# Performance work log

Hardware: AMD Instinct MI355X
Metric: run time of the kernel (lower is better)

## Reference

```python
import jax, jax.numpy as jnp
import numpy as np

N = 8192
SQUARE_SIZE = 10.0
NEIGHBOURHOOD = 1.0
THRESHOLD = 1.0
DECAY = 0.9


def setup_inputs() -> dict:
    key = jax.random.key(0)
    k1, k2, k3, k4 = jax.random.split(key, 4)
    # Random 2D topology on a square, as in SpikingLayer.__init__
    topo = jax.random.uniform(k1, (N, 2), dtype=jnp.float32) * SQUARE_SIZE
    # Pairwise squared distances without the [N,N,2] intermediate
    sq = jnp.sum(topo * topo, axis=1)  # [N]
    d2 = sq[:, None] + sq[None, :] - 2.0 * (topo @ topo.T)  # [N,N]
    mask = (d2 <= NEIGHBOURHOOD * NEIGHBOURHOOD).astype(jnp.float32)
    # Per-node weight rows, zeroed outside the neighbourhood radius
    W = jax.random.normal(k2, (N, N), dtype=jnp.float32) * mask
    # Random initial firing state (0/1) so dynamics are non-trivial
    f0 = (jax.random.uniform(k3, (N,)) > 0.5).astype(jnp.float32)
    v0 = jnp.zeros((N,), dtype=jnp.float32)
    x = jax.random.normal(k4, (N,), dtype=jnp.float32)  # unused, as in torch forward
    return {"W": W, "f0": f0, "v0": v0, "x": x, "num_steps": 64}


def reference(W, f0, v0, x, num_steps):
    # One scan step == one call to SpikingLayer.forward():
    #   node_x = W @ is_firing  (fused over all nodes)
    #   LIF update: v = decay*v + node_x; spike if v >= threshold; reset on spike
    def step(carry, _):
        v, f = carry
        u = W @ f                      # [N] weighted input from firing neighbours
        v = DECAY * v + u
        spike = v >= THRESHOLD         # bool [N]
        f_new = spike.astype(v.dtype)
        v = jnp.where(spike, 0.0, v)   # reset fired neurons
        return (v, f_new), f_new

    (_, _), firing_matrix = jax.lax.scan(step, (v0, f0), None, length=num_steps)
    return firing_matrix  # [num_steps, N], the accumulated firing_matrix
```

## Files before the change

kernel.cpp:

```cpp
#include <hip/hip_runtime.h>

#define NN 8192
#define STEPS 64
#define DECAYF 0.9f
#define THRESHF 1.0f
#define K_MAX 384
#define KITER2 (K_MAX / 32)

#define CBLOCKS 256
#define CTHREADS 1024
#define NWAVES 16
#define ROWS_PER_BLOCK 32

typedef unsigned long long u64;
typedef unsigned int u32;
typedef unsigned short u16;

__device__ __forceinline__ void pub_store(u64* p, u64 v) {
    __hip_atomic_store(p, v, __ATOMIC_RELAXED, __HIP_MEMORY_SCOPE_AGENT);
}
__device__ __forceinline__ u64 pub_load(const u64* p) {
    return __hip_atomic_load(p, __ATOMIC_RELAXED, __HIP_MEMORY_SCOPE_AGENT);
}

__global__ __launch_bounds__(CTHREADS) void spiking_all(
        const float* __restrict__ W,
        const float* __restrict__ f0,
        const float* __restrict__ v0,
        float* __restrict__ out,
        u64* __restrict__ fdata) {
    __shared__ u64 lds_pk[ROWS_PER_BLOCK * K_MAX];
    __shared__ u32 lds_fbits[2][CBLOCKS];
    __shared__ u32 lds_spike[NWAVES];
    __shared__ int lds_flag;
    __shared__ int lds_cnt[STEPS];

    const int tid  = threadIdx.x;
    const int wave = tid >> 6;
    const int lane = tid & 63;
    const int bid  = blockIdx.x;
    const u64 lmask = (1ull << lane) - 1ull;

    if (wave == 0) {
        float f = (lane < ROWS_PER_BLOCK) ? f0[bid * ROWS_PER_BLOCK + lane] : 0.0f;
        u64 m = __ballot(f != 0.0f);
        if (lane == 0)
            pub_store(&fdata[bid], (1ull << 32) | (u32)(m & 0xffffffffull));
    }

    for (int rr = 0; rr < 2; ++rr) {
        const int lr  = wave * 2 + rr;
        const int row = bid * ROWS_PER_BLOCK + lr;
        u64* pk = lds_pk + lr * K_MAX;
        for (int j = lane; j < K_MAX; j += 64) pk[j] = 0ull;
        const float4* wr4 = (const float4*)(W + (size_t)row * NN);
        int base = 0;
        for (int c4 = lane; c4 < NN / 4; c4 += 64) {
            float4 w = wr4[c4];
            const int col0 = c4 * 4;
            #pragma unroll
            for (int comp = 0; comp < 4; ++comp) {
                float val = (comp == 0) ? w.x : (comp == 1) ? w.y
                          : (comp == 2) ? w.z : w.w;
                u64 m = __ballot(val != 0.0f);
                if (val != 0.0f) {
                    int idx = base + __popcll(m & lmask);
                    if (idx < K_MAX)
                        pk[idx] = ((u64)(u32)(col0 + comp) << 32)
                                | (u64)__float_as_uint(val);
                }
                base += __popcll(m);
            }
        }
    }
    if (tid < STEPS) lds_cnt[tid] = 0;
    if (tid == 0) lds_flag = 0;

    const int lr   = wave * 2 + (lane >> 5);
    const int half = lane & 31;
    float vreg = v0[bid * ROWS_PER_BLOCK + lr];

    __syncthreads();

    for (int s = 0; s < STEPS; ++s) {
        if (wave == 0) {
            const u64* slot = fdata + (size_t)(s & 1) * CBLOCKS;
            const u32 want = (u32)(s + 1);
            u64 w0, w1, w2, w3;
            for (;;) {
                w0 = pub_load(&slot[lane]);
                w1 = pub_load(&slot[lane + 64]);
                w2 = pub_load(&slot[lane + 128]);
                w3 = pub_load(&slot[lane + 192]);
                int ok = ((u32)(w0 >> 32) == want) & ((u32)(w1 >> 32) == want)
                       & ((u32)(w2 >> 32) == want) & ((u32)(w3 >> 32) == want);
                if (__all(ok)) break;
            }
            u32* fb = lds_fbits[s & 1];
            fb[lane]       = (u32)w0;
            fb[lane + 64]  = (u32)w1;
            fb[lane + 128] = (u32)w2;
            fb[lane + 192] = (u32)w3;
            if (lane == 0)
                __hip_atomic_store(&lds_flag, s + 1, __ATOMIC_RELEASE,
                                   __HIP_MEMORY_SCOPE_WORKGROUP);
        } else {
            while (__hip_atomic_load(&lds_flag, __ATOMIC_ACQUIRE,
                                     __HIP_MEMORY_SCOPE_WORKGROUP) < s + 1)
                __builtin_amdgcn_s_sleep(1);
        }

        const u32* fb = lds_fbits[s & 1];
        const u64* pk = lds_pk + lr * K_MAX;

        double acc = 0.0;
        #pragma unroll
        for (int k = 0; k < KITER2; ++k) {
            const int j = half + (k << 5);
            u64 p   = pk[j];
            u32 c   = (u32)(p >> 32);
            float v = __uint_as_float((u32)p);
            u32 bit = (fb[c >> 5] >> (c & 31)) & 1u;
            acc += bit ? (double)v : 0.0;
        }
        #pragma unroll
        for (int m = 16; m >= 1; m >>= 1)
            acc += __shfl_xor(acc, m, 64);

        float u  = (float)acc;
        float vv = __fadd_rn(__fmul_rn(DECAYF, vreg), u);
        int fire = (vv >= THRESHF);
        vreg = fire ? 0.0f : vv;
        if (half == 0)
            out[(size_t)s * NN + bid * ROWS_PER_BLOCK + lr] = fire ? 1.0f : 0.0f;

        u64 bal = __ballot(fire);
        u32 bits2 = (u32)(bal & 1ull) | (u32)((bal >> 31) & 2ull);

        int old = -1;
        if (lane == 0) {
            __hip_atomic_store(&lds_spike[wave], bits2, __ATOMIC_RELAXED,
                               __HIP_MEMORY_SCOPE_WORKGROUP);
            old = __hip_atomic_fetch_add(&lds_cnt[s], 1, __ATOMIC_ACQ_REL,
                                         __HIP_MEMORY_SCOPE_WORKGROUP);
        }
        old = __shfl(old, 0, 64);
        if (old == NWAVES - 1) {
            u32 b = (lane < NWAVES) ? (lds_spike[lane] << (2 * lane)) : 0u;
            #pragma unroll
            for (int off = 8; off >= 1; off >>= 1)
                b |= __shfl_down(b, off, 64);
            if (lane == 0) {
                u64 word = ((u64)(u32)(s + 2) << 32) | b;
                pub_store(&fdata[(size_t)((s + 1) & 1) * CBLOCKS + bid], word);
            }
        }
    }
}

extern "C" void kernel_launch(void* const* d_in, const int* in_sizes, int n_in,
                              void* d_out, int out_size, void* d_ws, size_t ws_size,
                              hipStream_t stream) {
    const float* W  = (const float*)d_in[0];
    const float* f0 = (const float*)d_in[1];
    const float* v0 = (const float*)d_in[2];
    float* out = (float*)d_out;

    u64* fdata = (u64*)d_ws;

    spiking_all<<<dim3(CBLOCKS), dim3(CTHREADS), 0, stream>>>(W, f0, v0, out, fdata);
}
```

Before: 663.3 us.

## Split ELL extraction into separate kernel and hold sparse rows in registers

Moves the sparse-row extraction from the dense W matrix out of the persistent kernel into a separate kernel that is fully parallel over rows and writes a packed ELL array to the workspace. The persistent step kernel now uses 9 waves per block: one dedicated coordinator wave polls the global firing flags and publishes the block's spikes, and 8 compute waves each hold 4 rows' entries (24 per lane) in registers. This removes LDS staging of the packed entries and the per-step atomic counter election. The cost is an extra launch, a global round trip of the packed array, and a tighter coordinator-to-compute handshake through LDS.

```diff
diff --git a/kernel.cpp b/kernel.cpp
--- a/kernel.cpp
+++ b/kernel.cpp
@@ -5,16 +5,13 @@
 #define DECAYF 0.9f
 #define THRESHF 1.0f
 #define K_MAX 384
-#define KITER2 (K_MAX / 32)
+#define KITER 24
 
 #define CBLOCKS 256
-#define CTHREADS 1024
-#define NWAVES 16
-#define ROWS_PER_BLOCK 32
+#define STHREADS 576
 
 typedef unsigned long long u64;
 typedef unsigned int u32;
-typedef unsigned short u16;
 
 __device__ __forceinline__ void pub_store(u64* p, u64 v) {
     __hip_atomic_store(p, v, __ATOMIC_RELAXED, __HIP_MEMORY_SCOPE_AGENT);
@@ -23,67 +20,66 @@
     return __hip_atomic_load(p, __ATOMIC_RELAXED, __HIP_MEMORY_SCOPE_AGENT);
 }
 
-__global__ __launch_bounds__(CTHREADS) void spiking_all(
+__global__ __launch_bounds__(256) void extract_ell(
         const float* __restrict__ W,
+        u64* __restrict__ pk) {
+    const int wave = threadIdx.x >> 6;
+    const int lane = threadIdx.x & 63;
+    const int row  = blockIdx.x * 4 + wave;
+    const float4* wr4 = (const float4*)(W + (size_t)row * NN);
+    u64* pr = pk + (size_t)row * K_MAX;
+    const u64 lmask = (1ull << lane) - 1ull;
+
+    int base = 0;
+    for (int c4 = lane; c4 < NN / 4; c4 += 64) {
+        float4 w = wr4[c4];
+        const int col0 = c4 * 4;
+        #pragma unroll
+        for (int comp = 0; comp < 4; ++comp) {
+            float val = (comp == 0) ? w.x : (comp == 1) ? w.y
+                      : (comp == 2) ? w.z : w.w;
+            u64 m = __ballot(val != 0.0f);
+            if (val != 0.0f) {
+                int idx = base + __popcll(m & lmask);
+                if (idx < K_MAX)
+                    pr[idx] = ((u64)(u32)(col0 + comp) << 32)
+                            | (u64)__float_as_uint(val);
+            }
+            base += __popcll(m);
+        }
+    }
+    const int cap = (base < K_MAX) ? base : K_MAX;
+    for (int j = cap + lane; j < K_MAX; j += 64) pr[j] = 0ull;
+}
+
+__global__ __launch_bounds__(STHREADS) void spiking_steps(
+        const u64* __restrict__ pk,
         const float* __restrict__ f0,
         const float* __restrict__ v0,
         float* __restrict__ out,
         u64* __restrict__ fdata) {
-    __shared__ u64 lds_pk[ROWS_PER_BLOCK * K_MAX];
     __shared__ u32 lds_fbits[2][CBLOCKS];
-    __shared__ u32 lds_spike[NWAVES];
+    __shared__ u32 lds_spike[16];
     __shared__ int lds_flag;
-    __shared__ int lds_cnt[STEPS];
 
     const int tid  = threadIdx.x;
     const int wave = tid >> 6;
     const int lane = tid & 63;
     const int bid  = blockIdx.x;
-    const u64 lmask = (1ull << lane) - 1ull;
+
+    if (tid < 16) lds_spike[tid] = 0;
+    if (tid == 0) lds_flag = 0;
 
     if (wave == 0) {
-        float f = (lane < ROWS_PER_BLOCK) ? f0[bid * ROWS_PER_BLOCK + lane] : 0.0f;
+        float f = (lane < 32) ? f0[bid * 32 + lane] : 0.0f;
         u64 m = __ballot(f != 0.0f);
         if (lane == 0)
             pub_store(&fdata[bid], (1ull << 32) | (u32)(m & 0xffffffffull));
     }
-
-    for (int rr = 0; rr < 2; ++rr) {
-        const int lr  = wave * 2 + rr;
-        const int row = bid * ROWS_PER_BLOCK + lr;
-        u64* pk = lds_pk + lr * K_MAX;
-        for (int j = lane; j < K_MAX; j += 64) pk[j] = 0ull;
-        const float4* wr4 = (const float4*)(W + (size_t)row * NN);
-        int base = 0;
-        for (int c4 = lane; c4 < NN / 4; c4 += 64) {
-            float4 w = wr4[c4];
-            const int col0 = c4 * 4;
-            #pragma unroll
-            for (int comp = 0; comp < 4; ++comp) {
-                float val = (comp == 0) ? w.x : (comp == 1) ? w.y
-                          : (comp == 2) ? w.z : w.w;
-                u64 m = __ballot(val != 0.0f);
-                if (val != 0.0f) {
-                    int idx = base + __popcll(m & lmask);
-                    if (idx < K_MAX)
-                        pk[idx] = ((u64)(u32)(col0 + comp) << 32)
-                                | (u64)__float_as_uint(val);
-                }
-                base += __popcll(m);
-            }
-        }
-    }
-    if (tid < STEPS) lds_cnt[tid] = 0;
-    if (tid == 0) lds_flag = 0;
-
-    const int lr   = wave * 2 + (lane >> 5);
-    const int half = lane & 31;
-    float vreg = v0[bid * ROWS_PER_BLOCK + lr];
-
     __syncthreads();
 
-    for (int s = 0; s < STEPS; ++s) {
-        if (wave == 0) {
+    if (wave == 0) {
+        for (int s = 0; s < STEPS; ++s) {
             const u64* slot = fdata + (size_t)(s & 1) * CBLOCKS;
             const u32 want = (u32)(s + 1);
             u64 w0, w1, w2, w3;
@@ -104,55 +100,73 @@
             if (lane == 0)
                 __hip_atomic_store(&lds_flag, s + 1, __ATOMIC_RELEASE,
                                    __HIP_MEMORY_SCOPE_WORKGROUP);
-        } else {
+
+            u32 myw;
+            for (;;) {
+                myw = (lane < 8)
+                    ? __hip_atomic_load(&lds_spike[1 + lane], __ATOMIC_RELAXED,
+                                        __HIP_MEMORY_SCOPE_WORKGROUP)
+                    : (want << 8);
+                if (__all((myw >> 8) == want)) break;
+            }
+            u32 bits = (lane < 8) ? ((myw & 0xFu) << (lane * 4)) : 0u;
+            bits |= __shfl_xor(bits, 1, 64);
+            bits |= __shfl_xor(bits, 2, 64);
+            bits |= __shfl_xor(bits, 4, 64);
+            if (lane == 0)
+                pub_store(&fdata[(size_t)((s + 1) & 1) * CBLOCKS + bid],
+                          ((u64)(u32)(s + 2) << 32) | bits);
+        }
+    } else {
+        const int g    = wave - 1;
+        const int rloc = g * 4 + (lane >> 4);
+        const int row  = bid * 32 + rloc;
+        const int l16  = lane & 15;
+
+        u32 ecol[KITER]; float eval[KITER];
+        const u64* pr = pk + (size_t)row * K_MAX;
+        #pragma unroll
+        for (int k = 0; k < KITER; ++k) {
+            u64 p = pr[l16 + 16 * k];
+            ecol[k] = (u32)(p >> 32);
+            eval[k] = __uint_as_float((u32)p);
+        }
+        float vreg = v0[row];
+
+        for (int s = 0; s < STEPS; ++s) {
             while (__hip_atomic_load(&lds_flag, __ATOMIC_ACQUIRE,
                                      __HIP_MEMORY_SCOPE_WORKGROUP) < s + 1)
-                __builtin_amdgcn_s_sleep(1);
-        }
+                __builtin_amdgcn_s_sleep(2);
+            const u32* fb = lds_fbits[s & 1];
 
-        const u32* fb = lds_fbits[s & 1];
-        const u64* pk = lds_pk + lr * K_MAX;
+            double acc = 0.0;
+            #pragma unroll
+            for (int k = 0; k < KITER; ++k) {
+                u32 c = ecol[k];
+                u32 w = fb[c >> 5];
+                float sv = ((w >> (c & 31)) & 1u) ? eval[k] : 0.0f;
+                acc += (double)sv;
+            }
+            #pragma unroll
+            for (int m = 8; m >= 1; m >>= 1)
+                acc += __shfl_xor(acc, m, 64);
 
-        double acc = 0.0;
-        #pragma unroll
-        for (int k = 0; k < KITER2; ++k) {
-            const int j = half + (k << 5);
-            u64 p   = pk[j];
-            u32 c   = (u32)(p >> 32);
-            float v = __uint_as_float((u32)p);
-            u32 bit = (fb[c >> 5] >> (c & 31)) & 1u;
-            acc += bit ? (double)v : 0.0;
-        }
-        #pragma unroll
-        for (int m = 16; m >= 1; m >>= 1)
-            acc += __shfl_xor(acc, m, 64);
+            float u  = (float)acc;
+            float vv = __fadd_rn(__fmul_rn(DECAYF, vreg), u);
+            int fire = (vv >= THRESHF);
+            vreg = fire ? 0.0f : vv;
+            if (l16 == 0)
+                out[(size_t)s * NN + row] = fire ? 1.0f : 0.0f;
 
-        float u  = (float)acc;
-        float vv = __fadd_rn(__fmul_rn(DECAYF, vreg), u);
-        int fire = (vv >= THRESHF);
-        vreg = fire ? 0.0f : vv;
-        if (half == 0)
-            out[(size_t)s * NN + bid * ROWS_PER_BLOCK + lr] = fire ? 1.0f : 0.0f;
-
-        u64 bal = __ballot(fire);
-        u32 bits2 = (u32)(bal & 1ull) | (u32)((bal >> 31) & 2ull);
-
-        int old = -1;
-        if (lane == 0) {
-            __hip_atomic_store(&lds_spike[wave], bits2, __ATOMIC_RELAXED,
-                               __HIP_MEMORY_SCOPE_WORKGROUP);
-            old = __hip_atomic_fetch_add(&lds_cnt[s], 1, __ATOMIC_ACQ_REL,
-                                         __HIP_MEMORY_SCOPE_WORKGROUP);
-        }
-        old = __shfl(old, 0, 64);
-        if (old == NWAVES - 1) {
-            u32 b = (lane < NWAVES) ? (lds_spike[lane] << (2 * lane)) : 0u;
-            #pragma unroll
-            for (int off = 8; off >= 1; off >>= 1)
-                b |= __shfl_down(b, off, 64);
+            u64 bal = __ballot(fire);
             if (lane == 0) {
-                u64 word = ((u64)(u32)(s + 2) << 32) | b;
-                pub_store(&fdata[(size_t)((s + 1) & 1) * CBLOCKS + bid], word);
+                u32 bits4 = ((u32)(bal       ) & 1u)
+                          | (((u32)(bal >> 16) & 1u) << 1)
+                          | (((u32)(bal >> 32) & 1u) << 2)
+                          | (((u32)(bal >> 48) & 1u) << 3);
+                __hip_atomic_store(&lds_spike[1 + g],
+                                   ((u32)(s + 1) << 8) | bits4,
+                                   __ATOMIC_RELAXED, __HIP_MEMORY_SCOPE_WORKGROUP);
             }
         }
     }
@@ -166,7 +180,10 @@
     const float* v0 = (const float*)d_in[2];
     float* out = (float*)d_out;
 
-    u64* fdata = (u64*)d_ws;
+    u64* pk    = (u64*)d_ws;
+    u64* fdata = pk + (size_t)NN * K_MAX;
 
-    spiking_all<<<dim3(CBLOCKS), dim3(CTHREADS), 0, stream>>>(W, f0, v0, out, fdata);
+    extract_ell<<<dim3(NN / 4), dim3(256), 0, stream>>>(W, pk);
+    spiking_steps<<<dim3(CBLOCKS), dim3(STHREADS), 0, stream>>>(
+        pk, f0, v0, out, fdata);
 }
```

Measured after the change: 607.1 us. -8.5%, faster.
